# Optimization experiments

Hardware: AMD Instinct MI355X
Metric: run time of the kernel (lower is better)

Reference implementation:

```python
import jax, jax.numpy as jnp
import numpy as np

EMBED_DIM = 1024
NUM_HEADS = 16
HEAD_DIM = EMBED_DIM // NUM_HEADS
B, S = 2, 2048


def setup_inputs() -> dict:
    key = jax.random.key(0)
    ks = jax.random.split(key, 9)
    scale = 1.0 / np.sqrt(EMBED_DIM)
    return {
        "x": jax.random.normal(ks[0], (B, S, EMBED_DIM), dtype=jnp.float32),
        "Wq": jax.random.normal(ks[1], (EMBED_DIM, EMBED_DIM), dtype=jnp.float32) * scale,
        "bq": jnp.zeros((EMBED_DIM,), dtype=jnp.float32),
        "Wk": jax.random.normal(ks[2], (EMBED_DIM, EMBED_DIM), dtype=jnp.float32) * scale,
        "bk": jnp.zeros((EMBED_DIM,), dtype=jnp.float32),
        "Wv": jax.random.normal(ks[3], (EMBED_DIM, EMBED_DIM), dtype=jnp.float32) * scale,
        "bv": jnp.zeros((EMBED_DIM,), dtype=jnp.float32),
        "Wo": jax.random.normal(ks[4], (EMBED_DIM, EMBED_DIM), dtype=jnp.float32) * scale,
        "bo": jnp.zeros((EMBED_DIM,), dtype=jnp.float32),
    }


def _split_heads(t):
    # [B, S, E] -> [B, H, S, Dh]
    b, s, _ = t.shape
    return t.reshape(b, s, NUM_HEADS, HEAD_DIM).transpose(0, 2, 1, 3)


def reference(x, Wq, bq, Wk, bk, Wv, bv, Wo, bo):
    q = _split_heads(x @ Wq + bq)
    k = _split_heads(x @ Wk + bk)
    v = _split_heads(x @ Wv + bv)
    scale = jnp.sqrt(jnp.asarray(HEAD_DIM, dtype=x.dtype))
    scores = jnp.einsum("bhqd,bhkd->bhqk", q, k) / scale
    attn = jax.nn.softmax(scores, axis=-1)
    out = jnp.einsum("bhqk,bhkd->bhqd", attn, v)  # [B,H,S,Dh]
    out = out.transpose(0, 2, 1, 3).reshape(x.shape[0], x.shape[1], EMBED_DIM)
    return out @ Wo + bo
```

## Files before the change

### kernel.cpp

```cpp
#include <hip/hip_runtime.h>
#include <math.h>
#include <stdint.h>

typedef __bf16 bf16;
typedef __bf16 bf16x2 __attribute__((ext_vector_type(2)));
typedef __bf16 bf16x4 __attribute__((ext_vector_type(4)));
typedef __bf16 bf16x8 __attribute__((ext_vector_type(8)));
typedef float f32x4 __attribute__((ext_vector_type(4)));
typedef float f32x16 __attribute__((ext_vector_type(16)));

constexpr int E = 1024;
constexpr int S = 2048;
constexpr int H = 16;


__device__ __forceinline__ void gload16(const void* g, void* l) {
  __builtin_amdgcn_global_load_lds(
      (__attribute__((address_space(1))) void*)(uintptr_t)g,
      (__attribute__((address_space(3))) void*)(uint32_t)(uintptr_t)l, 16, 0, 0);
}

__device__ __forceinline__ f32x4 mfma16(bf16x8 a, bf16x8 b, f32x4 c) {
  return __builtin_amdgcn_mfma_f32_16x16x32_bf16(a, b, c, 0, 0, 0);
}
__device__ __forceinline__ f32x16 mfma32(bf16x8 a, bf16x8 b, f32x16 c) {
  return __builtin_amdgcn_mfma_f32_32x32x16_bf16(a, b, c, 0, 0, 0);
}

__device__ __forceinline__ float fexp2(float x) {
#if __has_builtin(__builtin_amdgcn_exp2f)
  return __builtin_amdgcn_exp2f(x);
#else
  float r;
  asm("v_exp_f32 %0, %1" : "=v"(r) : "v"(x));
  return r;
#endif
}

__device__ __forceinline__ uint32_t pkbf(float lo, float hi) {
  bf16x2 p;
  p[0] = (bf16)lo;
  p[1] = (bf16)hi;
  return __builtin_bit_cast(uint32_t, p);
}

__global__ __launch_bounds__(256) void cast_x(const float* __restrict__ x,
                                              bf16* __restrict__ o) {
  const size_t i = ((size_t)blockIdx.x * 256 + threadIdx.x) * 8;
  const float4 a = *(const float4*)(x + i);
  const float4 b = *(const float4*)(x + i + 4);
  bf16x8 r;
  r[0] = (bf16)a.x; r[1] = (bf16)a.y; r[2] = (bf16)a.z; r[3] = (bf16)a.w;
  r[4] = (bf16)b.x; r[5] = (bf16)b.y; r[6] = (bf16)b.z; r[7] = (bf16)b.w;
  *(bf16x8*)(o + i) = r;
}

__global__ __launch_bounds__(256) void transpose_cast_w(
    const float* __restrict__ W0, const float* __restrict__ W1,
    const float* __restrict__ W2, const float* __restrict__ W3,
    bf16* __restrict__ T0, bf16* __restrict__ T1, bf16* __restrict__ T2,
    bf16* __restrict__ T3) {
  const float* W;
  bf16* T;
  switch (blockIdx.z) {
    case 0: W = W0; T = T0; break;
    case 1: W = W1; T = T1; break;
    case 2: W = W2; T = T2; break;
    default: W = W3; T = T3; break;
  }
  __shared__ float t[64][65];
  const int k0 = blockIdx.y * 64, n0 = blockIdx.x * 64;
  const int tr = threadIdx.x >> 4;
  const int tc = (threadIdx.x & 15) * 4;
#pragma unroll
  for (int u = 0; u < 4; ++u) {
    const float4 v = *(const float4*)(W + (size_t)(k0 + tr + u * 16) * E + n0 + tc);
    t[tr + u * 16][tc + 0] = v.x;
    t[tr + u * 16][tc + 1] = v.y;
    t[tr + u * 16][tc + 2] = v.z;
    t[tr + u * 16][tc + 3] = v.w;
  }
  __syncthreads();
#pragma unroll
  for (int u = 0; u < 4; ++u) {
    const int n = tr + u * 16;
    bf16x4 o;
#pragma unroll
    for (int i = 0; i < 4; ++i) o[i] = (bf16)t[tc + i][n];
    *(bf16x4*)(T + (size_t)(n0 + n) * E + k0 + tc) = o;
  }
}

__global__ __launch_bounds__(256) void gemm_qkv(const bf16* __restrict__ A,
                                                const bf16* __restrict__ Wt,
                                                const float* __restrict__ bq,
                                                const float* __restrict__ bk,
                                                const float* __restrict__ bv,
                                                bf16* __restrict__ qo,
                                                bf16* __restrict__ ko,
                                                bf16* __restrict__ vo) {
  __shared__ __attribute__((aligned(16))) bf16 Asm[128 * 32];
  __shared__ __attribute__((aligned(16))) bf16 Bsm[128 * 32];
  const int z = blockIdx.z;
  const bf16* Bt = Wt + (size_t)z * E * E;
  const float* bias = (z == 0) ? bq : (z == 1) ? bk : bv;
  const int tid = threadIdx.x;
  const int w = tid >> 6, lane = tid & 63, quad = lane >> 4, ln = lane & 15;
  const int bm = blockIdx.y * 128, bn = blockIdx.x * 128;
  const int wr = w >> 1, wc = w & 1;
  const int srow = w * 32 + (lane >> 2);
  const int scol = (lane & 3) * 8;
  const bf16* Ag = A + (size_t)(bm + srow) * E + scol;
  const bf16* Bg = Bt + (size_t)(bn + srow) * E + scol;
  f32x4 acc[4][4] = {};

  for (int k0 = 0; k0 < E; k0 += 32) {
    gload16(Ag + k0, &Asm[(w * 32) * 32]);
    gload16(Ag + k0 + (size_t)16 * E, &Asm[(w * 32 + 16) * 32]);
    gload16(Bg + k0, &Bsm[(w * 32) * 32]);
    gload16(Bg + k0 + (size_t)16 * E, &Bsm[(w * 32 + 16) * 32]);
    __syncthreads();
    bf16x8 af[4], bfr[4];
#pragma unroll
    for (int t = 0; t < 4; ++t) {
      af[t] = *(const bf16x8*)&Asm[(wr * 64 + t * 16 + ln) * 32 + quad * 8];
      bfr[t] = *(const bf16x8*)&Bsm[(wc * 64 + t * 16 + ln) * 32 + quad * 8];
    }
#pragma unroll
    for (int rt = 0; rt < 4; ++rt)
#pragma unroll
      for (int ct = 0; ct < 4; ++ct)
        acc[rt][ct] = mfma16(af[rt], bfr[ct], acc[rt][ct]);
    __syncthreads();
  }

  const float scl = (z == 0) ? 0.18033688f : 1.0f;
  const int hglob = (bn + wc * 64) >> 6;
  float bvv[4];
#pragma unroll
  for (int ct = 0; ct < 4; ++ct) bvv[ct] = bias[bn + wc * 64 + ct * 16 + ln];

#pragma unroll
  for (int rt = 0; rt < 4; ++rt) {
    const int row0 = bm + wr * 64 + rt * 16 + quad * 4;
    const int bb = row0 >> 11;
    const int rl = row0 & 2047;
    const size_t hb = (size_t)(bb * 16 + hglob) * 131072;
#pragma unroll
    for (int ct = 0; ct < 4; ++ct) {
      if (z == 2) {
        const int mt = ct >> 1, ln32 = ((ct & 1) << 4) | ln;
        const int tau = rl >> 6, hfv = (rl >> 3) & 1, j0 = rl & 7;
        bf16x4 p;
#pragma unroll
        for (int r = 0; r < 4; ++r) p[r] = (bf16)(acc[rt][ct][r] + bvv[ct]);
        *(bf16x4*)&vo[hb + (size_t)((tau * 8 + mt * 4 + rt) * 512 +
                                    hfv * 256 + ln32 * 8 + j0)] = p;
      } else {
        bf16* o = (z == 0) ? qo : ko;
        const int t = rl >> 5, ln0 = rl & 31;
        const size_t base =
            hb + (size_t)((t * 4 + ct) * 512 + (ln >> 3) * 256 + (ln & 7));
#pragma unroll
        for (int r = 0; r < 4; ++r)
          o[base + (ln0 + r) * 8] = (bf16)((acc[rt][ct][r] + bvv[ct]) * scl);
      }
    }
  }
}

__global__ __launch_bounds__(256) void gemm_wo(const bf16* __restrict__ A,
                                               const bf16* __restrict__ Bt,
                                               const float* __restrict__ bias,
                                               float* __restrict__ C) {
  __shared__ __attribute__((aligned(16))) bf16 Asm[64 * 32];
  __shared__ __attribute__((aligned(16))) bf16 Bsm[128 * 32];
  const int tid = threadIdx.x;
  const int w = tid >> 6, lane = tid & 63, quad = lane >> 4, ln = lane & 15;
  const int bm = blockIdx.y * 64, bn = blockIdx.x * 128;
  const int wr = w >> 1, wc = w & 1;
  const int sr = lane >> 2, sc = (lane & 3) * 8;
  const bf16* Ag = A + (size_t)(bm + w * 16 + sr) * E + sc;
  const bf16* Bg = Bt + (size_t)(bn + w * 32 + sr) * E + sc;
  f32x4 acc[2][4] = {};

  for (int k0 = 0; k0 < E; k0 += 32) {
    gload16(Ag + k0, &Asm[(w * 16) * 32]);
    gload16(Bg + k0, &Bsm[(w * 32) * 32]);
    gload16(Bg + k0 + (size_t)16 * E, &Bsm[(w * 32 + 16) * 32]);
    __syncthreads();
    bf16x8 af[2], bfr[4];
#pragma unroll
    for (int t = 0; t < 2; ++t)
      af[t] = *(const bf16x8*)&Asm[(wr * 32 + t * 16 + ln) * 32 + quad * 8];
#pragma unroll
    for (int t = 0; t < 4; ++t)
      bfr[t] = *(const bf16x8*)&Bsm[(wc * 64 + t * 16 + ln) * 32 + quad * 8];
#pragma unroll
    for (int rt = 0; rt < 2; ++rt)
#pragma unroll
      for (int ct = 0; ct < 4; ++ct)
        acc[rt][ct] = mfma16(af[rt], bfr[ct], acc[rt][ct]);
    __syncthreads();
  }

  float bvv[4];
#pragma unroll
  for (int ct = 0; ct < 4; ++ct) bvv[ct] = bias[bn + wc * 64 + ct * 16 + ln];
#pragma unroll
  for (int rt = 0; rt < 2; ++rt) {
    const int row0 = bm + wr * 32 + rt * 16 + quad * 4;
#pragma unroll
    for (int ct = 0; ct < 4; ++ct) {
      const int c = bn + wc * 64 + ct * 16 + ln;
#pragma unroll
      for (int r = 0; r < 4; ++r)
        C[(size_t)(row0 + r) * E + c] = acc[rt][ct][r] + bvv[ct];
    }
  }
}

__global__ __launch_bounds__(512, 4) void attn_mfma(const bf16* __restrict__ Qf,
                                                    const bf16* __restrict__ Kf,
                                                    const bf16* __restrict__ Vf,
                                                    bf16* __restrict__ Og) {
  __shared__ __attribute__((aligned(16))) char smem[65536];

  const int tid = threadIdx.x;
  const int w = tid >> 6, lane = tid & 63, ln = lane & 31, hf = lane >> 5;
  const int qi = w & 3, ki = w >> 2;
  const int tq = blockIdx.x * 4 + qi;
  const int h = blockIdx.y, b = blockIdx.z;
  const size_t fb = (size_t)(b * H + h) * 131072;

  bf16x8 qf[4];
  {
    const bf16* qb = Qf + fb + (size_t)tq * 2048 + lane * 8;
#pragma unroll
    for (int c = 0; c < 4; ++c) qf[c] = *(const bf16x8*)(qb + c * 512);
  }

  const bf16* Ksrc = Kf + fb + qi * 1024 + lane * 8;
  const bf16* Vsrc = Vf + fb + qi * 1024 + lane * 8;
  const int dstoff = ki * 4096 + qi * 1024;

  float lpart = 0.f;
  f32x16 oacc[2] = {};

#define STAGE(i, buf)                                                  \
  do {                                                                 \
    const size_t toff = (size_t)(ki * 16 + (i)) * 4096;                \
    bf16* kd = (bf16*)(smem + (buf) * 32768) + dstoff;                 \
    bf16* vd = (bf16*)(smem + (buf) * 32768 + 16384) + dstoff;         \
    gload16(Ksrc + toff, kd);                                          \
    gload16(Ksrc + toff + 512, kd + 512);                              \
    gload16(Vsrc + toff, vd);                                          \
    gload16(Vsrc + toff + 512, vd + 512);                              \
  } while (0)

  STAGE(0, 0);
  __syncthreads();

#pragma unroll 2
  for (int i = 0; i < 16; ++i) {
    const int cur = i & 1;
    if (i < 15) STAGE(i + 1, cur ^ 1);
    const bf16* Ks = (const bf16*)(smem + cur * 32768) + ki * 4096;
    const bf16* Vs = (const bf16*)(smem + cur * 32768 + 16384) + ki * 4096;

#pragma unroll
    for (int mt = 0; mt < 2; ++mt) {
      f32x16 st = {};
      __builtin_amdgcn_s_setprio(1);
#pragma unroll
      for (int c = 0; c < 4; ++c)
        st = mfma32(*(const bf16x8*)&Ks[(mt * 4 + c) * 512 + lane * 8], qf[c],
                    st);
      __builtin_amdgcn_s_setprio(0);

      float pe[16];
#pragma unroll
      for (int r = 0; r < 16; ++r) pe[r] = fexp2(st[r]);
      lpart += (((pe[0] + pe[1]) + (pe[2] + pe[3])) +
                ((pe[4] + pe[5]) + (pe[6] + pe[7]))) +
               (((pe[8] + pe[9]) + (pe[10] + pe[11])) +
                ((pe[12] + pe[13]) + (pe[14] + pe[15])));

      bf16x8 pb[2];
#pragma unroll
      for (int cl = 0; cl < 2; ++cl) {
        uint32_t a01 = pkbf(pe[cl * 8 + 0], pe[cl * 8 + 1]);
        uint32_t a23 = pkbf(pe[cl * 8 + 2], pe[cl * 8 + 3]);
        uint32_t b01 = pkbf(pe[cl * 8 + 4], pe[cl * 8 + 5]);
        uint32_t b23 = pkbf(pe[cl * 8 + 6], pe[cl * 8 + 7]);
        auto r0 = __builtin_amdgcn_permlane32_swap(a01, b01, false, false);
        auto r1 = __builtin_amdgcn_permlane32_swap(a23, b23, false, false);
        union {
          bf16x8 v;
          uint32_t u[4];
        } pu;
        pu.u[0] = r0[0];
        pu.u[1] = r1[0];
        pu.u[2] = r0[1];
        pu.u[3] = r1[1];
        pb[cl] = pu.v;
      }

      __builtin_amdgcn_s_setprio(1);
#pragma unroll
      for (int vt = 0; vt < 2; ++vt) {
        oacc[vt] = mfma32(
            *(const bf16x8*)&Vs[(vt * 4 + mt * 2 + 0) * 512 + lane * 8], pb[0],
            oacc[vt]);
        oacc[vt] = mfma32(
            *(const bf16x8*)&Vs[(vt * 4 + mt * 2 + 1) * 512 + lane * 8], pb[1],
            oacc[vt]);
      }
      __builtin_amdgcn_s_setprio(0);
    }
    __syncthreads();
  }
#undef STAGE

  float* Ocmb = (float*)smem;
  float* Lcmb = (float*)(smem + 32768);
  if (ki == 1) {
#pragma unroll
    for (int vt = 0; vt < 2; ++vt)
#pragma unroll
      for (int r = 0; r < 16; ++r)
        Ocmb[qi * 2048 + (vt * 16 + r) * 64 + lane] = oacc[vt][r];
    Lcmb[qi * 64 + lane] = lpart;
  }
  __syncthreads();
  if (ki == 0) {
#pragma unroll
    for (int vt = 0; vt < 2; ++vt)
#pragma unroll
      for (int r = 0; r < 16; ++r)
        oacc[vt][r] += Ocmb[qi * 2048 + (vt * 16 + r) * 64 + lane];
    lpart += Lcmb[qi * 64 + lane];

    lpart += __shfl_xor(lpart, 32);
    const float inv = 1.0f / lpart;

    bf16* orow = Og + ((size_t)b * S + (size_t)tq * 32 + ln) * E + h * 64;
#pragma unroll
    for (int vt = 0; vt < 2; ++vt) {
#pragma unroll
      for (int g = 0; g < 4; ++g) {
        bf16x4 o;
#pragma unroll
        for (int j = 0; j < 4; ++j) o[j] = (bf16)(oacc[vt][g * 4 + j] * inv);
        *(bf16x4*)&orow[vt * 32 + g * 8 + hf * 4] = o;
      }
    }
  }
}

extern "C" void kernel_launch(void* const* d_in, const int* in_sizes, int n_in,
                              void* d_out, int out_size, void* d_ws, size_t ws_size,
                              hipStream_t stream) {
  const float* x = (const float*)d_in[0];
  const float* Wq = (const float*)d_in[1];
  const float* bq = (const float*)d_in[2];
  const float* Wk = (const float*)d_in[3];
  const float* bk = (const float*)d_in[4];
  const float* Wv = (const float*)d_in[5];
  const float* bv = (const float*)d_in[6];
  const float* Wo = (const float*)d_in[7];
  const float* bo = (const float*)d_in[8];

  const size_t ME = (size_t)4096 * 1024;
  const size_t WE = (size_t)1024 * 1024;
  bf16* xb = (bf16*)d_ws;
  bf16* wqt = xb + ME;
  bf16* wkt = wqt + WE;
  bf16* wvt = wkt + WE;
  bf16* wot = wvt + WE;
  bf16* qb = wot + WE;
  bf16* kb = qb + ME;
  bf16* vt = kb + ME;
  bf16* ab = vt + ME;

  cast_x<<<2048, 256, 0, stream>>>(x, xb);
  transpose_cast_w<<<dim3(16, 16, 4), 256, 0, stream>>>(Wq, Wk, Wv, Wo, wqt, wkt,
                                                        wvt, wot);
  gemm_qkv<<<dim3(8, 32, 3), 256, 0, stream>>>(xb, wqt, bq, bk, bv, qb, kb, vt);
  attn_mfma<<<dim3(S / 128, H, 2), 512, 0, stream>>>(qb, kb, vt, ab);
  gemm_wo<<<dim3(8, 64), 256, 0, stream>>>(ab, wot, bo, (float*)d_out);
}
```

Baseline: 191.3 us.

## Rewrite QKV GEMM with 256x256 tiles, double-buffered async loads and swizzled LDS

Replaces the 128x128 single-buffered QKV GEMM with a 512-thread kernel that computes 256x256 tiles over the concatenated Q/K/V weights. Global-to-LDS loads are double-buffered and interleaved with MFMA phases, controlled by explicit vmcnt waits, barriers and setprio. LDS addresses use an XOR swizzle to avoid bank conflicts, and the block order is remapped to improve L2 reuse. The aim is to hide memory latency and raise arithmetic intensity. In exchange it uses 128KB of LDS, which caps occupancy, and launches only 192 blocks, which may leave some CUs idle.

New measurement: 200.7 us. +4.9%, slower.

```diff
diff --git a/kernel.cpp b/kernel.cpp
--- a/kernel.cpp
+++ b/kernel.cpp
@@ -91,79 +91,157 @@
   }
 }
 
-__global__ __launch_bounds__(256) void gemm_qkv(const bf16* __restrict__ A,
-                                                const bf16* __restrict__ Wt,
-                                                const float* __restrict__ bq,
-                                                const float* __restrict__ bk,
-                                                const float* __restrict__ bv,
-                                                bf16* __restrict__ qo,
-                                                bf16* __restrict__ ko,
-                                                bf16* __restrict__ vo) {
-  __shared__ __attribute__((aligned(16))) bf16 Asm[128 * 32];
-  __shared__ __attribute__((aligned(16))) bf16 Bsm[128 * 32];
-  const int z = blockIdx.z;
-  const bf16* Bt = Wt + (size_t)z * E * E;
+__global__ __launch_bounds__(512, 2) void gemm_qkv(const bf16* __restrict__ A,
+                                                   const bf16* __restrict__ Wt,
+                                                   const float* __restrict__ bq,
+                                                   const float* __restrict__ bk,
+                                                   const float* __restrict__ bv,
+                                                   bf16* __restrict__ qo,
+                                                   bf16* __restrict__ ko,
+                                                   bf16* __restrict__ vo) {
+  __shared__ __attribute__((aligned(16))) char smem[131072];
+  const int tid = threadIdx.x;
+  const int lane = tid & 63, quad = lane >> 4, ln = lane & 15;
+  const int wid = tid >> 6, wr = wid >> 2, wc = wid & 3;
+
+  const int id = blockIdx.x + 12 * blockIdx.y;
+  const int sw = (id & 7) * 24 + (id >> 3);
+  const int bx = sw % 12, by = sw / 12;
+  const int bm = by * 256, bn = bx * 256;
+  const int z = bx >> 2;
+
+  const int r0 = tid >> 3;
+  const int csw = ((tid & 7) * 8) ^ (((r0 >> 2) & 1) << 4);
+  const bf16* Ag0 = A + (size_t)bm * E;
+  const bf16* Bg0 = Wt + (size_t)bn * E;
+
+#define STG(srcp, dd, boff, h, kt)                                            \
+  do {                                                                        \
+    const bf16* s_ = (srcp) + (size_t)((h) * 128 + r0) * E + (kt) * 64 + csw; \
+    char* d_ = smem + (dd) * 65536 + (boff) + (h) * 16384 + tid * 16;         \
+    gload16(s_, d_);                                                          \
+    gload16(s_ + (size_t)64 * E, d_ + 8192);                                  \
+  } while (0)
+
+  const int sx = ((ln >> 2) & 1) << 5;
+  const int lnq = ln * 128 + quad * 16;
+  const int bB = (wc & 1) * 8192 + lnq;
+  const char* Ab0 = smem + wr * 16384;
+  const char* Bb0 = smem + 32768 + (wc >> 1) * 16384;
+
+  f32x4 acc[8][4] = {};
+
+  STG(Ag0, 0, 0, 0, 0);
+  STG(Ag0, 0, 0, 1, 0);
+  STG(Bg0, 0, 32768, 0, 0);
+  STG(Bg0, 0, 32768, 1, 0);
+  STG(Bg0, 1, 32768, 0, 1);
+  STG(Bg0, 1, 32768, 1, 1);
+  asm volatile("s_waitcnt vmcnt(4)" ::: "memory");
+  __builtin_amdgcn_s_barrier();
+
+  for (int j = 0; j < 8; ++j) {
+    const int kt0 = 2 * j, kt1 = 2 * j + 1;
+    bf16x8 bfr[4][2];
+#pragma unroll
+    for (int p = 0; p < 8; ++p) {
+      const int d = p >> 2, q = p & 3;
+      const char* Ab = Ab0 + d * 65536;
+      const char* Bb = Bb0 + d * 65536;
+
+      if (q == 0) {
+#pragma unroll
+        for (int nf = 0; nf < 4; ++nf)
+#pragma unroll
+          for (int ks = 0; ks < 2; ++ks)
+            bfr[nf][ks] =
+                *(const bf16x8*)(Bb + ((bB + nf * 2048 + ks * 64) ^ sx));
+      }
+      bf16x8 afr[2][2];
+#pragma unroll
+      for (int m2 = 0; m2 < 2; ++m2)
+#pragma unroll
+        for (int ks = 0; ks < 2; ++ks)
+          afr[m2][ks] = *(const bf16x8*)(
+              Ab + ((lnq + (q * 2 + m2) * 2048 + ks * 64) ^ sx));
+
+      if (p == 0) {
+        STG(Ag0, 1, 0, 0, kt1);
+      } else if (p == 1) {
+        STG(Ag0, 1, 0, 1, kt1);
+        if (kt0 + 2 < 16) STG(Bg0, 0, 32768, 0, kt0 + 2);
+      } else if (p == 2) {
+        if (kt0 + 2 < 16) STG(Bg0, 0, 32768, 1, kt0 + 2);
+      } else if (p == 4) {
+        if (kt0 + 2 < 16) STG(Ag0, 0, 0, 0, kt0 + 2);
+      } else if (p == 5) {
+        if (kt0 + 2 < 16) STG(Ag0, 0, 0, 1, kt0 + 2);
+      } else if (p == 6) {
+        if (kt1 + 2 < 16) STG(Bg0, 1, 32768, 0, kt1 + 2);
+      } else if (p == 7) {
+        if (kt1 + 2 < 16) STG(Bg0, 1, 32768, 1, kt1 + 2);
+      }
+
+      if (q == 3) {
+        if (p == 3) {
+          if (j < 7)
+            asm volatile("s_waitcnt vmcnt(4)" ::: "memory");
+          else
+            asm volatile("s_waitcnt vmcnt(0)" ::: "memory");
+        } else {
+          if (j < 7) asm volatile("s_waitcnt vmcnt(4)" ::: "memory");
+        }
+      }
+
+      __builtin_amdgcn_s_barrier();
+      asm volatile("s_waitcnt lgkmcnt(0)" ::: "memory");
+      __builtin_amdgcn_sched_barrier(0);
+      __builtin_amdgcn_s_setprio(1);
+#pragma unroll
+      for (int m2 = 0; m2 < 2; ++m2)
+#pragma unroll
+        for (int nf = 0; nf < 4; ++nf) {
+          acc[q * 2 + m2][nf] = mfma16(afr[m2][0], bfr[nf][0], acc[q * 2 + m2][nf]);
+          acc[q * 2 + m2][nf] = mfma16(afr[m2][1], bfr[nf][1], acc[q * 2 + m2][nf]);
+        }
+      __builtin_amdgcn_s_setprio(0);
+      __builtin_amdgcn_s_barrier();
+    }
+  }
+#undef STG
+
   const float* bias = (z == 0) ? bq : (z == 1) ? bk : bv;
-  const int tid = threadIdx.x;
-  const int w = tid >> 6, lane = tid & 63, quad = lane >> 4, ln = lane & 15;
-  const int bm = blockIdx.y * 128, bn = blockIdx.x * 128;
-  const int wr = w >> 1, wc = w & 1;
-  const int srow = w * 32 + (lane >> 2);
-  const int scol = (lane & 3) * 8;
-  const bf16* Ag = A + (size_t)(bm + srow) * E + scol;
-  const bf16* Bg = Bt + (size_t)(bn + srow) * E + scol;
-  f32x4 acc[4][4] = {};
-
-  for (int k0 = 0; k0 < E; k0 += 32) {
-    gload16(Ag + k0, &Asm[(w * 32) * 32]);
-    gload16(Ag + k0 + (size_t)16 * E, &Asm[(w * 32 + 16) * 32]);
-    gload16(Bg + k0, &Bsm[(w * 32) * 32]);
-    gload16(Bg + k0 + (size_t)16 * E, &Bsm[(w * 32 + 16) * 32]);
-    __syncthreads();
-    bf16x8 af[4], bfr[4];
-#pragma unroll
-    for (int t = 0; t < 4; ++t) {
-      af[t] = *(const bf16x8*)&Asm[(wr * 64 + t * 16 + ln) * 32 + quad * 8];
-      bfr[t] = *(const bf16x8*)&Bsm[(wc * 64 + t * 16 + ln) * 32 + quad * 8];
-    }
-#pragma unroll
-    for (int rt = 0; rt < 4; ++rt)
-#pragma unroll
-      for (int ct = 0; ct < 4; ++ct)
-        acc[rt][ct] = mfma16(af[rt], bfr[ct], acc[rt][ct]);
-    __syncthreads();
-  }
-
   const float scl = (z == 0) ? 0.18033688f : 1.0f;
-  const int hglob = (bn + wc * 64) >> 6;
+  const int hglob = (bx & 3) * 4 + wc;
   float bvv[4];
 #pragma unroll
-  for (int ct = 0; ct < 4; ++ct) bvv[ct] = bias[bn + wc * 64 + ct * 16 + ln];
-
-#pragma unroll
-  for (int rt = 0; rt < 4; ++rt) {
-    const int row0 = bm + wr * 64 + rt * 16 + quad * 4;
+  for (int nf = 0; nf < 4; ++nf)
+    bvv[nf] = bias[(bn + wc * 64 + nf * 16 + ln) & 1023];
+
+#pragma unroll
+  for (int mf = 0; mf < 8; ++mf) {
+    const int row0 = bm + wr * 128 + mf * 16 + quad * 4;
     const int bb = row0 >> 11;
     const int rl = row0 & 2047;
     const size_t hb = (size_t)(bb * 16 + hglob) * 131072;
 #pragma unroll
-    for (int ct = 0; ct < 4; ++ct) {
+    for (int nf = 0; nf < 4; ++nf) {
       if (z == 2) {
-        const int mt = ct >> 1, ln32 = ((ct & 1) << 4) | ln;
+        const int mt = nf >> 1, ln32 = ((nf & 1) << 4) | ln;
         const int tau = rl >> 6, hfv = (rl >> 3) & 1, j0 = rl & 7;
-        bf16x4 p;
-#pragma unroll
-        for (int r = 0; r < 4; ++r) p[r] = (bf16)(acc[rt][ct][r] + bvv[ct]);
-        *(bf16x4*)&vo[hb + (size_t)((tau * 8 + mt * 4 + rt) * 512 +
-                                    hfv * 256 + ln32 * 8 + j0)] = p;
+        bf16x4 pp;
+#pragma unroll
+        for (int r = 0; r < 4; ++r) pp[r] = (bf16)(acc[mf][nf][r] + bvv[nf]);
+        *(bf16x4*)&vo[hb + (size_t)((tau * 8 + mt * 4 + (mf & 3)) * 512 +
+                                    hfv * 256 + ln32 * 8 + j0)] = pp;
       } else {
         bf16* o = (z == 0) ? qo : ko;
         const int t = rl >> 5, ln0 = rl & 31;
         const size_t base =
-            hb + (size_t)((t * 4 + ct) * 512 + (ln >> 3) * 256 + (ln & 7));
+            hb + (size_t)((t * 4 + nf) * 512 + (ln >> 3) * 256 + (ln & 7));
 #pragma unroll
         for (int r = 0; r < 4; ++r)
-          o[base + (ln0 + r) * 8] = (bf16)((acc[rt][ct][r] + bvv[ct]) * scl);
+          o[base + (ln0 + r) * 8] = (bf16)((acc[mf][nf][r] + bvv[nf]) * scl);
       }
     }
   }
@@ -386,7 +464,7 @@
   cast_x<<<2048, 256, 0, stream>>>(x, xb);
   transpose_cast_w<<<dim3(16, 16, 4), 256, 0, stream>>>(Wq, Wk, Wv, Wo, wqt, wkt,
                                                         wvt, wot);
-  gemm_qkv<<<dim3(8, 32, 3), 256, 0, stream>>>(xb, wqt, bq, bk, bv, qb, kb, vt);
+  gemm_qkv<<<dim3(12, 16), 512, 0, stream>>>(xb, wqt, bq, bk, bv, qb, kb, vt);
   attn_mfma<<<dim3(S / 128, H, 2), 512, 0, stream>>>(qb, kb, vt, ab);
   gemm_wo<<<dim3(8, 64), 256, 0, stream>>>(ab, wot, bo, (float*)d_out);
 }
```
